# Kernel optimization log

Measured on AMD Instinct MI355X. Metric: run time of the kernel, lower is better.

## Reference

```python
import jax, jax.numpy as jnp
import numpy as np

B, N, D, K = 16, 1024, 512, 8
NUM_ITERS = 3
EPS = 1e-08
LN_EPS = 1e-05


def layer_norm(x, g, b):
    m = jnp.mean(x, axis=-1, keepdims=True)
    v = jnp.var(x, axis=-1, keepdims=True)
    return (x - m) * jax.lax.rsqrt(v + LN_EPS) * g + b


def setup_inputs() -> dict:
    key = jax.random.key(0)
    ks = jax.random.split(key, 8)
    s = 1.0 / np.sqrt(D)
    return {
        "embeddings": jax.random.normal(ks[0], (B, N, D), jnp.float32),
        "noise_init": jax.random.normal(ks[1], (B, K, D), jnp.float32),
        "noise_final": jax.random.normal(ks[2], (B, K, D), jnp.float32),
        "slots_mu": jax.random.normal(ks[3], (1, K, D), jnp.float32) * s,
        "slots_logsigma": jax.random.normal(ks[4], (1, K, D), jnp.float32) * s,
        "mixing_coeffs": jnp.ones((1, K), jnp.float32) / K,
        "Wk": jax.random.normal(ks[5], (D, D), jnp.float32) * s,
        "bk": jnp.zeros((D,), jnp.float32),
        "Wq": jax.random.normal(ks[6], (D, D), jnp.float32) * s,
        "bq": jnp.zeros((D,), jnp.float32),
        "Wv": jax.random.normal(ks[7], (D, D), jnp.float32) * s,
        "bv": jnp.zeros((D,), jnp.float32),
        "ln_g": jnp.ones((D,), jnp.float32),
        "ln_b": jnp.zeros((D,), jnp.float32),
    }


def reference(embeddings, noise_init, noise_final, slots_mu, slots_logsigma,
              mixing_coeffs, Wk, bk, Wq, bq, Wv, bv, ln_g, ln_b):
    b, n, d = embeddings.shape
    mixing = jnp.broadcast_to(mixing_coeffs, (b, K))           # [B,K]
    mu = jnp.broadcast_to(slots_mu, (b, K, d))                 # [B,K,D]
    sigma = jnp.exp(jnp.broadcast_to(slots_logsigma, (b, K, d)))
    slots = mu + sigma * noise_init                            # sampled slots

    x = layer_norm(embeddings, ln_g, ln_b)
    keys = x @ Wk + bk                                         # [B,N,D]
    values = x @ Wv + bv                                       # [B,N,D]
    # slots are never updated inside the loop, so queries are loop-invariant
    queries = slots @ Wq + bq                                  # [B,K,D]

    log2pi = jnp.float32(np.log(2.0 * np.pi))
    attn = None
    for _ in range(NUM_ITERS):
        diff = keys[:, :, None, :] - queries[:, None, :, :]    # [B,N,K,D]
        gll = -0.5 * jnp.sum(diff * diff / (sigma[:, None] ** 2 + EPS), axis=-1)  # [B,N,K]
        gll = (-0.5 * d * log2pi
               - 0.5 * jnp.sum(jnp.log(jnp.abs(sigma) + EPS), axis=-1)[:, None, :]
               + gll)
        attn = mixing[:, None, :] * gll                        # [B,N,K]
        attn = attn / jnp.sum(attn, axis=-1, keepdims=True)
        attn = attn / (jnp.sum(attn, axis=1, keepdims=True) + EPS)
        mu = jnp.einsum('bnk,bnd->bkd', attn, values)          # [B,K,D]
        diff2 = values[:, :, None, :] - mu[:, None, :, :]      # [B,N,K,D]
        sigma = jnp.einsum('bnk,bnkd->bkd', attn, diff2 * diff2)
        mixing = jnp.sum(attn, axis=1) / n

    sigma = jnp.maximum(jnp.abs(sigma), EPS)
    slots = mu + sigma * noise_final
    return slots, jnp.transpose(attn, (0, 2, 1))
```

## Files before the change

kernel.cpp:

```cpp
#include <hip/hip_runtime.h>
#include <math.h>

#define BB 16
#define NN 1024
#define DD 512
#define KK 8
#define EPS_ 1e-8f
#define LN_EPS_ 1e-5f
#define GLL_C0 (-470.4965290007924f)

typedef __attribute__((ext_vector_type(8))) short short8;
typedef __attribute__((ext_vector_type(4))) short short4v;
typedef __attribute__((ext_vector_type(4))) float f32x4;
typedef __attribute__((ext_vector_type(4))) int int4v;

static __device__ inline short f2bf(float f) {
    unsigned u = __builtin_bit_cast(unsigned, f);
    u = (u + 0x7fff + ((u >> 16) & 1)) >> 16;
    return (short)u;
}
static __device__ inline float bf2f(short s) {
    unsigned u = ((unsigned)(unsigned short)s) << 16;
    return __builtin_bit_cast(float, u);
}

struct Params {
    const float *emb, *noise_init, *noise_final, *slots_mu, *slots_logsg,
                *mixing_co, *Wk, *bk, *Wq, *bq, *Wv, *bv, *ln_g, *ln_b;
    float *out;
    float *queries, *attn, *s1p, *s2p, *off, *mix16, *colsum;
    short *Abf, *E, *Vbf, *WtKV, *WqT, *slotbf, *F_bt;
};

__global__ __launch_bounds__(256) void k_pre(Params p)
{
    __shared__ __align__(16) short eb[4352];
    int u = blockIdx.x, tid = threadIdx.x;
    if (u < 4096) {
        int row  = u * 4 + (tid >> 6);
        int lane = tid & 63;
        const float* e = p.emb + (size_t)row * DD + lane * 8;
        float4 v0 = *(const float4*)e;
        float4 v1 = *(const float4*)(e + 4);
        float v[8] = {v0.x, v0.y, v0.z, v0.w, v1.x, v1.y, v1.z, v1.w};
        float s = 0.0f;
#pragma unroll
        for (int j = 0; j < 8; j++) s += v[j];
#pragma unroll
        for (int off = 32; off; off >>= 1) s += __shfl_xor(s, off);
        float m = s * (1.0f / DD);
        float vs = 0.0f;
#pragma unroll
        for (int j = 0; j < 8; j++) { float d = v[j] - m; vs = fmaf(d, d, vs); }
#pragma unroll
        for (int off = 32; off; off >>= 1) vs += __shfl_xor(vs, off);
        float rstd = rsqrtf(vs * (1.0f / DD) + LN_EPS_);

        float4 g0 = *(const float4*)&p.ln_g[lane * 8];
        float4 g1 = *(const float4*)&p.ln_g[lane * 8 + 4];
        float4 b0 = *(const float4*)&p.ln_b[lane * 8];
        float4 b1 = *(const float4*)&p.ln_b[lane * 8 + 4];
        float g[8] = {g0.x, g0.y, g0.z, g0.w, g1.x, g1.y, g1.z, g1.w};
        float bb[8] = {b0.x, b0.y, b0.z, b0.w, b1.x, b1.y, b1.z, b1.w};
        short8 o;
#pragma unroll
        for (int j = 0; j < 8; j++) o[j] = f2bf(fmaf((v[j] - m) * rstd, g[j], bb[j]));
        *(short8*)&p.Abf[(size_t)row * DD + lane * 8] = o;
    } else if (u < 4864) {
        int idx = u - 4096;
        int z = idx >> 8, rem = idx & 255;
        const float* W = (z == 0) ? p.Wk : (z == 1) ? p.Wv : p.Wq;
        short* T; int nbase;
        if (z < 2) { T = p.WtKV; nbase = z * 512; } else { T = p.WqT; nbase = 0; }
        int k0 = (rem & 15) * 32, n0 = (rem >> 4) * 32;
        int tx = tid & 31, ty = tid >> 5;
        float (*t)[33] = (float (*)[33])eb;
#pragma unroll
        for (int q = 0; q < 4; q++)
            t[ty + q * 8][tx] = W[(size_t)(k0 + ty + q * 8) * DD + n0 + tx];
        __syncthreads();
#pragma unroll
        for (int q = 0; q < 4; q++)
            T[(size_t)(nbase + n0 + ty + q * 8) * DD + k0 + tx] = f2bf(t[tx][ty + q * 8]);
    } else {
        int idx = u - 4864;
        int b = idx >> 3, k = idx & 7;
#pragma unroll
        for (int q = 0; q < 2; q++) {
            int d = tid + q * 256;
            float sg = expf(p.slots_logsg[k * DD + d]);
            float sl = fmaf(sg, p.noise_init[((size_t)(b * KK + k)) * DD + d],
                            p.slots_mu[k * DD + d]);
            p.slotbf[((size_t)(b * KK + k)) * DD + d] = f2bf(sl);
        }
    }
}

__global__ __launch_bounds__(256) void k_gemm(Params p)
{
    __shared__ __align__(16) short smem[16384];
    int u = blockIdx.x, tid = threadIdx.x;
    int w = tid >> 6, l = tid & 63;
    int x, by, qmode;
    if (u >= 1024) { qmode = 1; x = u - 1024; if (x >= 4) return; by = 128; }
    else           { qmode = 0; x = u >> 7;   by = u & 127; }
    const short* A  = qmode ? p.slotbf : p.Abf + (size_t)by * 128 * DD;
    const short* Bt = qmode ? p.WqT : p.WtKV;
    int row0 = qmode ? 0 : by * 128;
    int col0 = x * 128;

    short* As = smem;
    short* Bs = smem + 8192;
    int sr = l >> 3;
    int sg_off = ((l & 7) ^ sr) * 8;
    int mq = (w & 1) * 64, nq = (w >> 1) * 64;
    int fr = l & 15;
    int orow = (l >> 4) * 4, ocol = l & 15;

    int4v ra[4], rb4[4];
    auto LOADR = [&](int k0) {
#pragma unroll
        for (int j = 0; j < 4; j++) {
            int rbj = w * 32 + j * 8;
            int r   = rbj + sr;
            ra[j]  = *(const int4v*)(A  + (size_t)r * DD + k0 + sg_off);
            rb4[j] = *(const int4v*)(Bt + (size_t)(col0 + r) * DD + k0 + sg_off);
        }
    };
    auto WRITES = [&]() {
#pragma unroll
        for (int j = 0; j < 4; j++) {
            int rbj = w * 32 + j * 8;
            *(int4v*)&As[rbj * 64 + l * 8] = ra[j];
            *(int4v*)&Bs[rbj * 64 + l * 8] = rb4[j];
        }
    };

    f32x4 acc[4][4] = {};
    LOADR(0);
    WRITES();
    __syncthreads();
    for (int i = 0; i < 8; i++) {
        if (i < 7) LOADR((i + 1) * 64);
#pragma unroll
        for (int kk = 0; kk < 2; kk++) {
            int g = kk * 4 + (l >> 4);
            short8 af[4], bfv[4];
#pragma unroll
            for (int mi = 0; mi < 4; mi++)
                af[mi] = *(const short8*)&As[(mq + mi * 16 + fr) * 64 + (g ^ (fr & 7)) * 8];
#pragma unroll
            for (int ni = 0; ni < 4; ni++)
                bfv[ni] = *(const short8*)&Bs[(nq + ni * 16 + fr) * 64 + (g ^ (fr & 7)) * 8];
#pragma unroll
            for (int mi = 0; mi < 4; mi++)
#pragma unroll
                for (int ni = 0; ni < 4; ni++)
                    acc[mi][ni] = __builtin_amdgcn_mfma_f32_16x16x32_bf16(
                        af[mi], bfv[ni], acc[mi][ni], 0, 0, 0);
        }
        __syncthreads();
        if (i < 7) {
            WRITES();
            __syncthreads();
        }
    }

    float bvv[4];
#pragma unroll
    for (int ni = 0; ni < 4; ni++) {
        int col = col0 + nq + ni * 16 + ocol;
        bvv[ni] = qmode ? p.bq[col] : (x < 4 ? p.bk[col] : p.bv[col - 512]);
    }

    if (qmode) {
#pragma unroll
        for (int ni = 0; ni < 4; ni++) {
            int col = col0 + nq + ni * 16 + ocol;
#pragma unroll
            for (int mi = 0; mi < 4; mi++)
#pragma unroll
                for (int r = 0; r < 4; r++)
                    p.queries[(size_t)(mq + mi * 16 + orow + r) * DD + col] =
                        acc[mi][ni][r] + bvv[ni];
        }
    } else {
        short* eb = smem;
        int npass = (x < 4) ? 2 : 1;
        for (int pass = 0; pass < npass; pass++) {
#pragma unroll
            for (int mi = 0; mi < 4; mi++)
#pragma unroll
                for (int r = 0; r < 4; r++) {
                    int row = mq + mi * 16 + orow + r;
                    int sw = ((row >> 2) & 3) << 1;
#pragma unroll
                    for (int ni = 0; ni < 4; ni++) {
                        int colg = nq + ni * 16 + ocol;
                        float val = acc[mi][ni][r] + bvv[ni];
                        if (x < 4 && pass == 0) val = val * val;
                        eb[row * 128 + (((colg >> 3) ^ sw) * 8) + (colg & 7)] = f2bf(val);
                    }
                }
            __syncthreads();
#pragma unroll
            for (int i = 0; i < 8; i++) {
                int row = i * 16 + w * 4 + (l >> 4);
                int c = l & 15;
                int cc = c ^ (((row >> 2) & 3) << 1);
                short8 vv = *(const short8*)&eb[row * 128 + cc * 8];
                if (x < 4) {
                    size_t a = (size_t)(row0 + row) * 1024 +
                               (pass ? 512 + col0 : col0) + c * 8;
                    *(short8*)&p.E[a] = vv;
                } else {
                    *(short8*)&p.Vbf[(size_t)(row0 + row) * 512 +
                                     (col0 - 512) + c * 8] = vv;
                }
            }
            __syncthreads();
        }
    }
}

__global__ __launch_bounds__(256) void k_fprep0(Params p)
{
    __shared__ float red[512];
    int u = blockIdx.x, tid = threadIdx.x;
    int b = u >> 4, k = u & 15;
    short* Fr = p.F_bt + (size_t)(b * 16 + k) * 1024;
    if (k >= KK) {
        short4v zv = {0, 0, 0, 0};
        *(short4v*)&Fr[tid * 4] = zv;
        if (tid == 0) { p.off[b * 16 + k] = 0.0f; p.mix16[b * 16 + k] = 0.0f; }
        return;
    }
    float* rc = red;
    float* rl = red + 256;
    float c = 0.0f, ld = 0.0f;
#pragma unroll
    for (int q = 0; q < 2; q++) {
        int d = tid * 2 + q;
        float sg = expf(p.slots_logsg[k * DD + d]);
        float iv = 1.0f / (sg * sg + EPS_);
        float qv = p.queries[((size_t)(b * KK + k)) * DD + d];
        Fr[d]       = f2bf(-0.5f * iv);
        Fr[512 + d] = f2bf(qv * iv);
        c  = fmaf(qv * qv, iv, c);
        ld += logf(fabsf(sg) + EPS_);
    }
    rc[tid] = c; rl[tid] = ld;
    __syncthreads();
    for (int s = 128; s > 0; s >>= 1) {
        if (tid < s) { rc[tid] += rc[tid + s]; rl[tid] += rl[tid + s]; }
        __syncthreads();
    }
    if (tid == 0) {
        p.off[b * 16 + k]    = GLL_C0 - 0.5f * rl[0] - 0.5f * rc[0];
        p.mix16[b * 16 + k]  = p.mixing_co[k];
        p.colsum[b * KK + k] = 0.0f;
    }
}

__global__ __launch_bounds__(256) void k_gllmu(Params p)
{
    __shared__ f32x4 red[2][64];
    __shared__ float asml[32 * KK];
    int u = blockIdx.x, tid = threadIdx.x;
    int w = tid >> 6, l = tid & 63;
    int b = u >> 5, chunk = u & 31;
    int n0 = chunk * 32;
    int t = w & 1, khalf = w >> 1;

    const short* Ea = p.E + ((size_t)(b * NN + n0 + t * 16 + (l & 15))) * 1024
                      + khalf * 512 + (l >> 4) * 8;
    const short* Fa = p.F_bt + (size_t)(b * 16 + (l & 15)) * 1024
                      + khalf * 512 + (l >> 4) * 8;
    f32x4 acc0 = {}, acc1 = {};
#pragma unroll
    for (int j = 0; j < 8; j++) {
        short8 a0 = *(const short8*)&Ea[j * 64];
        short8 f0 = *(const short8*)&Fa[j * 64];
        acc0 = __builtin_amdgcn_mfma_f32_16x16x32_bf16(a0, f0, acc0, 0, 0, 0);
        short8 a1 = *(const short8*)&Ea[j * 64 + 32];
        short8 f1 = *(const short8*)&Fa[j * 64 + 32];
        acc1 = __builtin_amdgcn_mfma_f32_16x16x32_bf16(a1, f1, acc1, 0, 0, 0);
    }
    f32x4 acc = acc0 + acc1;

    if (khalf) red[t][l] = acc;
    __syncthreads();
    if (!khalf) {
        acc += red[t][l];
        int col = l & 15;
        int rloc = t * 16 + (l >> 4) * 4;
        float offv = p.off[b * 16 + col];
        float mixv = p.mix16[b * 16 + col];
        float a[4], den[4];
#pragma unroll
        for (int r = 0; r < 4; r++) {
            a[r] = mixv * (acc[r] + offv);
            den[r] = a[r];
        }
#pragma unroll
        for (int mask = 1; mask <= 8; mask <<= 1)
#pragma unroll
            for (int r = 0; r < 4; r++) den[r] += __shfl_xor(den[r], mask);
        float csl = 0.0f;
        if (col < KK) {
#pragma unroll
            for (int r = 0; r < 4; r++) {
                float vv = a[r] / den[r];
                asml[(rloc + r) * KK + col] = vv;
                p.attn[((size_t)(b * NN + n0 + rloc + r)) * KK + col] = vv;
                csl += vv;
            }
        }
        csl += __shfl_xor(csl, 16);
        csl += __shfl_xor(csl, 32);
        if (l < KK) atomicAdd(&p.colsum[b * KK + l], csl);
    }
    __syncthreads();

    int d0 = tid * 2;
    float s1[2][KK] = {}, s2[2][KK] = {};
    const short* vb = p.Vbf + ((size_t)(b * NN + n0)) * DD + d0;
#pragma unroll 4
    for (int nn = 0; nn < 32; nn++) {
        short2 vs = *(const short2*)&vb[(size_t)nn * DD];
        float v0 = bf2f(vs.x), v1 = bf2f(vs.y);
        float v0q = v0 * v0, v1q = v1 * v1;
        float4 a0 = *(const float4*)&asml[nn * KK];
        float4 a1 = *(const float4*)&asml[nn * KK + 4];
        float aa[8] = {a0.x, a0.y, a0.z, a0.w, a1.x, a1.y, a1.z, a1.w};
#pragma unroll
        for (int k = 0; k < KK; k++) {
            s1[0][k] = fmaf(aa[k], v0, s1[0][k]);
            s2[0][k] = fmaf(aa[k], v0q, s2[0][k]);
            s1[1][k] = fmaf(aa[k], v1, s1[1][k]);
            s2[1][k] = fmaf(aa[k], v1q, s2[1][k]);
        }
    }
    size_t base = ((size_t)(b * 32 + chunk) * KK) * DD + d0;
#pragma unroll
    for (int k = 0; k < KK; k++) {
        *(float2*)&p.s1p[base + (size_t)k * DD] = make_float2(s1[0][k], s1[1][k]);
        *(float2*)&p.s2p[base + (size_t)k * DD] = make_float2(s2[0][k], s2[1][k]);
    }
}

__global__ __launch_bounds__(256) void k_fprep(Params p)
{
    __shared__ float red[512];
    int u = blockIdx.x, tid = threadIdx.x;
    int b = u >> 3, k = u & 7;
    float cs   = p.colsum[b * KK + k];
    float inv  = 1.0f / (cs + EPS_);
    float ssum = cs * inv;
    short* Fr = p.F_bt + (size_t)(b * 16 + k) * 1024;
    float* rc = red;
    float* rl = red + 256;
    float c = 0.0f, ld = 0.0f;
#pragma unroll
    for (int q = 0; q < 2; q++) {
        int d = tid * 2 + q;
        float s1 = 0.0f, s2 = 0.0f;
#pragma unroll
        for (int ns = 0; ns < 32; ns++) {
            size_t o = ((size_t)(b * 32 + ns) * KK + k) * DD + d;
            s1 += p.s1p[o];
            s2 += p.s2p[o];
        }
        float m  = s1 * inv;
        float sg = s2 * inv - m * m * (2.0f - ssum);
        float iv = 1.0f / (sg * sg + EPS_);
        float qv = p.queries[((size_t)(b * KK + k)) * DD + d];
        Fr[d]       = f2bf(-0.5f * iv);
        Fr[512 + d] = f2bf(qv * iv);
        c  = fmaf(qv * qv, iv, c);
        ld += logf(fabsf(sg) + EPS_);
    }
    rc[tid] = c; rl[tid] = ld;
    __syncthreads();
    for (int s = 128; s > 0; s >>= 1) {
        if (tid < s) { rc[tid] += rc[tid + s]; rl[tid] += rl[tid + s]; }
        __syncthreads();
    }
    if (tid == 0) {
        p.off[b * 16 + k]    = GLL_C0 - 0.5f * rl[0] - 0.5f * rc[0];
        p.mix16[b * 16 + k]  = ssum * (1.0f / NN);
        p.colsum[b * KK + k] = 0.0f;
    }
}

__global__ __launch_bounds__(256) void k_final(Params p)
{
    int u = blockIdx.x, tid = threadIdx.x;
    if (u < 256) {
        int gid = u * 256 + tid;
        int d = gid & 511;
        int k = (gid >> 9) & 7;
        int b = gid >> 12;
        float s1 = 0.0f, s2 = 0.0f;
#pragma unroll
        for (int ns = 0; ns < 32; ns++) {
            size_t o = ((size_t)(b * 32 + ns) * KK + k) * DD + d;
            s1 += p.s1p[o];
            s2 += p.s2p[o];
        }
        float cs   = p.colsum[b * KK + k];
        float inv  = 1.0f / (cs + EPS_);
        float ssum = cs * inv;
        float m    = s1 * inv;
        float sg   = s2 * inv - m * m * (2.0f - ssum);
        p.out[gid] = fmaf(fmaxf(fabsf(sg), EPS_), p.noise_final[gid], m);
    } else {
        int gid = (u - 256) * 256 + tid;
        int b = gid >> 13;
        int k = (gid >> 10) & 7;
        int n = gid & 1023;
        float cs = p.colsum[b * KK + k];
        p.out[BB * KK * DD + gid] =
            p.attn[((size_t)(b * NN + n)) * KK + k] / (cs + EPS_);
    }
}

extern "C" void kernel_launch(void* const* d_in, const int* in_sizes, int n_in,
                              void* d_out, int out_size, void* d_ws, size_t ws_size,
                              hipStream_t stream)
{
    Params pp;
    pp.emb         = (const float*)d_in[0];
    pp.noise_init  = (const float*)d_in[1];
    pp.noise_final = (const float*)d_in[2];
    pp.slots_mu    = (const float*)d_in[3];
    pp.slots_logsg = (const float*)d_in[4];
    pp.mixing_co   = (const float*)d_in[5];
    pp.Wk          = (const float*)d_in[6];
    pp.bk          = (const float*)d_in[7];
    pp.Wq          = (const float*)d_in[8];
    pp.bq          = (const float*)d_in[9];
    pp.Wv          = (const float*)d_in[10];
    pp.bv          = (const float*)d_in[11];
    pp.ln_g        = (const float*)d_in[12];
    pp.ln_b        = (const float*)d_in[13];
    pp.out         = (float*)d_out;

    float* ws = (float*)d_ws;
    pp.queries = ws;
    pp.attn    = pp.queries + BB * KK * DD;
    pp.s1p     = pp.attn + BB * NN * KK;
    pp.s2p     = pp.s1p + (size_t)BB * 32 * KK * DD;
    pp.off     = pp.s2p + (size_t)BB * 32 * KK * DD;
    pp.mix16   = pp.off + BB * 16;
    pp.colsum  = pp.mix16 + BB * 16;
    pp.Abf     = (short*)(pp.colsum + BB * KK);
    pp.E       = pp.Abf + (size_t)BB * NN * DD;
    pp.Vbf     = pp.E + (size_t)BB * NN * 1024;
    pp.WtKV    = pp.Vbf + (size_t)BB * NN * DD;
    pp.WqT     = pp.WtKV + (size_t)1024 * DD;
    pp.slotbf  = pp.WqT + (size_t)DD * DD;
    pp.F_bt    = pp.slotbf + (size_t)BB * KK * DD;

    k_pre<<<4992, 256, 0, stream>>>(pp);
    k_gemm<<<1032, 256, 0, stream>>>(pp);
    k_fprep0<<<256, 256, 0, stream>>>(pp);
    for (int it = 0; it < 3; it++) {
        k_gllmu<<<512, 256, 0, stream>>>(pp);
        if (it < 2) k_fprep<<<128, 256, 0, stream>>>(pp);
    }
    k_final<<<768, 256, 0, stream>>>(pp);
}
```

Baseline: 229.8 us.

## Store keys once and square them in the GLL kernel; load GEMM fragments directly

The GEMM no longer writes an expanded [K^2 | K] bf16 buffer. It writes only K, and the GLL kernel squares the loaded key fragments in registers before the MFMA. This halves the key-side writes and the reads repeated across the three iterations. The GEMM main loop also drops LDS staging and barriers, loading MFMA fragments straight from global memory with register double buffering. The direct loads are uncoalesced 16-byte row reads and may rely on cache hits. Squaring a bf16-rounded key adds a little rounding difference.

```diff
diff --git a/kernel.cpp b/kernel.cpp
--- a/kernel.cpp
+++ b/kernel.cpp
@@ -12,7 +12,6 @@
 typedef __attribute__((ext_vector_type(8))) short short8;
 typedef __attribute__((ext_vector_type(4))) short short4v;
 typedef __attribute__((ext_vector_type(4))) float f32x4;
-typedef __attribute__((ext_vector_type(4))) int int4v;
 
 static __device__ inline short f2bf(float f) {
     unsigned u = __builtin_bit_cast(unsigned, f);
@@ -29,7 +28,7 @@
                 *mixing_co, *Wk, *bk, *Wq, *bq, *Wv, *bv, *ln_g, *ln_b;
     float *out;
     float *queries, *attn, *s1p, *s2p, *off, *mix16, *colsum;
-    short *Abf, *E, *Vbf, *WtKV, *WqT, *slotbf, *F_bt;
+    short *Abf, *Kbf, *Vbf, *WtKV, *WqT, *slotbf, *F_bt;
 };
 
 __global__ __launch_bounds__(256) void k_pre(Params p)
@@ -98,7 +97,7 @@
 
 __global__ __launch_bounds__(256) void k_gemm(Params p)
 {
-    __shared__ __align__(16) short smem[16384];
+    __shared__ __align__(16) short eb[128 * 128];
     int u = blockIdx.x, tid = threadIdx.x;
     int w = tid >> 6, l = tid & 63;
     int x, by, qmode;
@@ -109,61 +108,39 @@
     int row0 = qmode ? 0 : by * 128;
     int col0 = x * 128;
 
-    short* As = smem;
-    short* Bs = smem + 8192;
-    int sr = l >> 3;
-    int sg_off = ((l & 7) ^ sr) * 8;
     int mq = (w & 1) * 64, nq = (w >> 1) * 64;
     int fr = l & 15;
     int orow = (l >> 4) * 4, ocol = l & 15;
 
-    int4v ra[4], rb4[4];
-    auto LOADR = [&](int k0) {
-#pragma unroll
-        for (int j = 0; j < 4; j++) {
-            int rbj = w * 32 + j * 8;
-            int r   = rbj + sr;
-            ra[j]  = *(const int4v*)(A  + (size_t)r * DD + k0 + sg_off);
-            rb4[j] = *(const int4v*)(Bt + (size_t)(col0 + r) * DD + k0 + sg_off);
-        }
-    };
-    auto WRITES = [&]() {
-#pragma unroll
-        for (int j = 0; j < 4; j++) {
-            int rbj = w * 32 + j * 8;
-            *(int4v*)&As[rbj * 64 + l * 8] = ra[j];
-            *(int4v*)&Bs[rbj * 64 + l * 8] = rb4[j];
-        }
-    };
-
+    const short* Abase = A + (size_t)(mq + fr) * DD + (l >> 4) * 8;
+    const short* Bbase = Bt + (size_t)(col0 + nq + fr) * DD + (l >> 4) * 8;
+
+    short8 af[2][4], bf[2][4];
     f32x4 acc[4][4] = {};
-    LOADR(0);
-    WRITES();
-    __syncthreads();
-    for (int i = 0; i < 8; i++) {
-        if (i < 7) LOADR((i + 1) * 64);
-#pragma unroll
-        for (int kk = 0; kk < 2; kk++) {
-            int g = kk * 4 + (l >> 4);
-            short8 af[4], bfv[4];
+
+#pragma unroll
+    for (int mi = 0; mi < 4; mi++) af[0][mi] = *(const short8*)(Abase + (size_t)mi * 16 * DD);
+#pragma unroll
+    for (int ni = 0; ni < 4; ni++) bf[0][ni] = *(const short8*)(Bbase + (size_t)ni * 16 * DD);
+
+#pragma unroll
+    for (int ks = 0; ks < 16; ks++) {
+        int cur = ks & 1;
+        if (ks < 15) {
+            int ko = (ks + 1) * 32;
 #pragma unroll
             for (int mi = 0; mi < 4; mi++)
-                af[mi] = *(const short8*)&As[(mq + mi * 16 + fr) * 64 + (g ^ (fr & 7)) * 8];
+                af[cur ^ 1][mi] = *(const short8*)(Abase + (size_t)mi * 16 * DD + ko);
 #pragma unroll
             for (int ni = 0; ni < 4; ni++)
-                bfv[ni] = *(const short8*)&Bs[(nq + ni * 16 + fr) * 64 + (g ^ (fr & 7)) * 8];
-#pragma unroll
-            for (int mi = 0; mi < 4; mi++)
-#pragma unroll
-                for (int ni = 0; ni < 4; ni++)
-                    acc[mi][ni] = __builtin_amdgcn_mfma_f32_16x16x32_bf16(
-                        af[mi], bfv[ni], acc[mi][ni], 0, 0, 0);
-        }
-        __syncthreads();
-        if (i < 7) {
-            WRITES();
-            __syncthreads();
-        }
+                bf[cur ^ 1][ni] = *(const short8*)(Bbase + (size_t)ni * 16 * DD + ko);
+        }
+#pragma unroll
+        for (int mi = 0; mi < 4; mi++)
+#pragma unroll
+            for (int ni = 0; ni < 4; ni++)
+                acc[mi][ni] = __builtin_amdgcn_mfma_f32_16x16x32_bf16(
+                    af[cur][mi], bf[cur][ni], acc[mi][ni], 0, 0, 0);
     }
 
     float bvv[4];
@@ -185,40 +162,29 @@
                         acc[mi][ni][r] + bvv[ni];
         }
     } else {
-        short* eb = smem;
-        int npass = (x < 4) ? 2 : 1;
-        for (int pass = 0; pass < npass; pass++) {
-#pragma unroll
-            for (int mi = 0; mi < 4; mi++)
-#pragma unroll
-                for (int r = 0; r < 4; r++) {
-                    int row = mq + mi * 16 + orow + r;
-                    int sw = ((row >> 2) & 3) << 1;
-#pragma unroll
-                    for (int ni = 0; ni < 4; ni++) {
-                        int colg = nq + ni * 16 + ocol;
-                        float val = acc[mi][ni][r] + bvv[ni];
-                        if (x < 4 && pass == 0) val = val * val;
-                        eb[row * 128 + (((colg >> 3) ^ sw) * 8) + (colg & 7)] = f2bf(val);
-                    }
-                }
-            __syncthreads();
-#pragma unroll
-            for (int i = 0; i < 8; i++) {
-                int row = i * 16 + w * 4 + (l >> 4);
-                int c = l & 15;
-                int cc = c ^ (((row >> 2) & 3) << 1);
-                short8 vv = *(const short8*)&eb[row * 128 + cc * 8];
-                if (x < 4) {
-                    size_t a = (size_t)(row0 + row) * 1024 +
-                               (pass ? 512 + col0 : col0) + c * 8;
-                    *(short8*)&p.E[a] = vv;
-                } else {
-                    *(short8*)&p.Vbf[(size_t)(row0 + row) * 512 +
-                                     (col0 - 512) + c * 8] = vv;
+        short* dst = (x < 4) ? p.Kbf : p.Vbf;
+        int ccol0 = (x & 3) * 128;
+#pragma unroll
+        for (int mi = 0; mi < 4; mi++)
+#pragma unroll
+            for (int r = 0; r < 4; r++) {
+                int row = mq + mi * 16 + orow + r;
+                int sw = ((row >> 2) & 3) << 1;
+#pragma unroll
+                for (int ni = 0; ni < 4; ni++) {
+                    int colg = nq + ni * 16 + ocol;
+                    eb[row * 128 + (((colg >> 3) ^ sw) * 8) + (colg & 7)] =
+                        f2bf(acc[mi][ni][r] + bvv[ni]);
                 }
             }
-            __syncthreads();
+        __syncthreads();
+#pragma unroll
+        for (int i = 0; i < 8; i++) {
+            int row = i * 16 + w * 4 + (l >> 4);
+            int c = l & 15;
+            int cc = c ^ (((row >> 2) & 3) << 1);
+            short8 vv = *(const short8*)&eb[row * 128 + cc * 8];
+            *(short8*)&dst[(size_t)(row0 + row) * 512 + ccol0 + c * 8] = vv;
         }
     }
 }
@@ -272,19 +238,24 @@
     int n0 = chunk * 32;
     int t = w & 1, khalf = w >> 1;
 
-    const short* Ea = p.E + ((size_t)(b * NN + n0 + t * 16 + (l & 15))) * 1024
-                      + khalf * 512 + (l >> 4) * 8;
-    const short* Fa = p.F_bt + (size_t)(b * 16 + (l & 15)) * 1024
-                      + khalf * 512 + (l >> 4) * 8;
+    const short* Ka = p.Kbf + ((size_t)(b * NN + n0 + t * 16 + (l & 15))) * 512
+                      + khalf * 256 + (l >> 4) * 8;
+    const short* Fi = p.F_bt + (size_t)(b * 16 + (l & 15)) * 1024
+                      + khalf * 256 + (l >> 4) * 8;
     f32x4 acc0 = {}, acc1 = {};
 #pragma unroll
     for (int j = 0; j < 8; j++) {
-        short8 a0 = *(const short8*)&Ea[j * 64];
-        short8 f0 = *(const short8*)&Fa[j * 64];
-        acc0 = __builtin_amdgcn_mfma_f32_16x16x32_bf16(a0, f0, acc0, 0, 0, 0);
-        short8 a1 = *(const short8*)&Ea[j * 64 + 32];
-        short8 f1 = *(const short8*)&Fa[j * 64 + 32];
-        acc1 = __builtin_amdgcn_mfma_f32_16x16x32_bf16(a1, f1, acc1, 0, 0, 0);
+        short8 kf = *(const short8*)&Ka[j * 32];
+        short8 f0 = *(const short8*)&Fi[j * 32];
+        short8 f1 = *(const short8*)&Fi[j * 32 + 512];
+        short8 k2;
+#pragma unroll
+        for (int e = 0; e < 8; e++) {
+            float kv = bf2f(kf[e]);
+            k2[e] = f2bf(kv * kv);
+        }
+        acc0 = __builtin_amdgcn_mfma_f32_16x16x32_bf16(k2, f0, acc0, 0, 0, 0);
+        acc1 = __builtin_amdgcn_mfma_f32_16x16x32_bf16(kf, f1, acc1, 0, 0, 0);
     }
     f32x4 acc = acc0 + acc1;
 
@@ -455,8 +426,8 @@
     pp.mix16   = pp.off + BB * 16;
     pp.colsum  = pp.mix16 + BB * 16;
     pp.Abf     = (short*)(pp.colsum + BB * KK);
-    pp.E       = pp.Abf + (size_t)BB * NN * DD;
-    pp.Vbf     = pp.E + (size_t)BB * NN * 1024;
+    pp.Kbf     = pp.Abf + (size_t)BB * NN * DD;
+    pp.Vbf     = pp.Kbf + (size_t)BB * NN * DD;
     pp.WtKV    = pp.Vbf + (size_t)BB * NN * DD;
     pp.WqT     = pp.WtKV + (size_t)1024 * DD;
     pp.slotbf  = pp.WqT + (size_t)DD * DD;
```

Result: slower. 250.5 us (+9.0%).

## Store keys once in bf16 and square them on the fly in the GLL kernel

Applied to the files above, without the earlier changes.

The GEMM epilogue now writes only the bf16 keys (512 columns) instead of an interleaved [k^2, k] buffer of 1024 columns. The key square is recomputed inside k_gllmu from the loaded bf16 key before the MFMA. This halves the key buffer written by the GEMM and read in each of the three iterations. k_gllmu also moves to 512 threads: four waves split the D dimension, with a three-way shared-memory reduction, and the mu/sigma accumulation uses one column per thread. Squaring the already-rounded bf16 key adds a small precision change, plus extra ALU conversion work per load.

```diff
diff --git a/kernel.cpp b/kernel.cpp
--- a/kernel.cpp
+++ b/kernel.cpp
@@ -29,7 +29,7 @@
                 *mixing_co, *Wk, *bk, *Wq, *bq, *Wv, *bv, *ln_g, *ln_b;
     float *out;
     float *queries, *attn, *s1p, *s2p, *off, *mix16, *colsum;
-    short *Abf, *E, *Vbf, *WtKV, *WqT, *slotbf, *F_bt;
+    short *Abf, *Kbf, *Vbf, *WtKV, *WqT, *slotbf, *F_bt;
 };
 
 __global__ __launch_bounds__(256) void k_pre(Params p)
@@ -186,39 +186,29 @@
         }
     } else {
         short* eb = smem;
-        int npass = (x < 4) ? 2 : 1;
-        for (int pass = 0; pass < npass; pass++) {
-#pragma unroll
-            for (int mi = 0; mi < 4; mi++)
-#pragma unroll
-                for (int r = 0; r < 4; r++) {
-                    int row = mq + mi * 16 + orow + r;
-                    int sw = ((row >> 2) & 3) << 1;
-#pragma unroll
-                    for (int ni = 0; ni < 4; ni++) {
-                        int colg = nq + ni * 16 + ocol;
-                        float val = acc[mi][ni][r] + bvv[ni];
-                        if (x < 4 && pass == 0) val = val * val;
-                        eb[row * 128 + (((colg >> 3) ^ sw) * 8) + (colg & 7)] = f2bf(val);
-                    }
-                }
-            __syncthreads();
-#pragma unroll
-            for (int i = 0; i < 8; i++) {
-                int row = i * 16 + w * 4 + (l >> 4);
-                int c = l & 15;
-                int cc = c ^ (((row >> 2) & 3) << 1);
-                short8 vv = *(const short8*)&eb[row * 128 + cc * 8];
-                if (x < 4) {
-                    size_t a = (size_t)(row0 + row) * 1024 +
-                               (pass ? 512 + col0 : col0) + c * 8;
-                    *(short8*)&p.E[a] = vv;
-                } else {
-                    *(short8*)&p.Vbf[(size_t)(row0 + row) * 512 +
-                                     (col0 - 512) + c * 8] = vv;
+        short* dst = (x < 4) ? p.Kbf : p.Vbf;
+        int ccol0 = (x & 3) * 128;
+#pragma unroll
+        for (int mi = 0; mi < 4; mi++)
+#pragma unroll
+            for (int r = 0; r < 4; r++) {
+                int row = mq + mi * 16 + orow + r;
+                int sw = ((row >> 2) & 3) << 1;
+#pragma unroll
+                for (int ni = 0; ni < 4; ni++) {
+                    int colg = nq + ni * 16 + ocol;
+                    eb[row * 128 + (((colg >> 3) ^ sw) * 8) + (colg & 7)] =
+                        f2bf(acc[mi][ni][r] + bvv[ni]);
                 }
             }
-            __syncthreads();
+        __syncthreads();
+#pragma unroll
+        for (int i = 0; i < 8; i++) {
+            int row = i * 16 + w * 4 + (l >> 4);
+            int c = l & 15;
+            int cc = c ^ (((row >> 2) & 3) << 1);
+            short8 vv = *(const short8*)&eb[row * 128 + cc * 8];
+            *(short8*)&dst[(size_t)(row0 + row) * 512 + ccol0 + c * 8] = vv;
         }
     }
 }
@@ -262,36 +252,42 @@
     }
 }
 
-__global__ __launch_bounds__(256) void k_gllmu(Params p)
-{
-    __shared__ f32x4 red[2][64];
+__global__ __launch_bounds__(512) void k_gllmu(Params p)
+{
+    __shared__ f32x4 red[3][2][64];
     __shared__ float asml[32 * KK];
     int u = blockIdx.x, tid = threadIdx.x;
     int w = tid >> 6, l = tid & 63;
     int b = u >> 5, chunk = u & 31;
     int n0 = chunk * 32;
-    int t = w & 1, khalf = w >> 1;
-
-    const short* Ea = p.E + ((size_t)(b * NN + n0 + t * 16 + (l & 15))) * 1024
-                      + khalf * 512 + (l >> 4) * 8;
-    const short* Fa = p.F_bt + (size_t)(b * 16 + (l & 15)) * 1024
-                      + khalf * 512 + (l >> 4) * 8;
+    int t = w & 1, ks = w >> 1;
+
+    const short* Ka = p.Kbf + ((size_t)(b * NN + n0 + t * 16 + (l & 15))) * 512
+                      + ks * 128 + (l >> 4) * 8;
+    const short* Fi = p.F_bt + (size_t)(b * 16 + (l & 15)) * 1024
+                      + ks * 128 + (l >> 4) * 8;
     f32x4 acc0 = {}, acc1 = {};
 #pragma unroll
-    for (int j = 0; j < 8; j++) {
-        short8 a0 = *(const short8*)&Ea[j * 64];
-        short8 f0 = *(const short8*)&Fa[j * 64];
-        acc0 = __builtin_amdgcn_mfma_f32_16x16x32_bf16(a0, f0, acc0, 0, 0, 0);
-        short8 a1 = *(const short8*)&Ea[j * 64 + 32];
-        short8 f1 = *(const short8*)&Fa[j * 64 + 32];
-        acc1 = __builtin_amdgcn_mfma_f32_16x16x32_bf16(a1, f1, acc1, 0, 0, 0);
+    for (int j = 0; j < 4; j++) {
+        short8 kf = *(const short8*)&Ka[j * 32];
+        short8 f0 = *(const short8*)&Fi[j * 32];
+        short8 f1 = *(const short8*)&Fi[j * 32 + 512];
+        short8 k2;
+#pragma unroll
+        for (int e = 0; e < 8; e++) {
+            float kv = bf2f(kf[e]);
+            k2[e] = f2bf(kv * kv);
+        }
+        acc0 = __builtin_amdgcn_mfma_f32_16x16x32_bf16(k2, f0, acc0, 0, 0, 0);
+        acc1 = __builtin_amdgcn_mfma_f32_16x16x32_bf16(kf, f1, acc1, 0, 0, 0);
     }
     f32x4 acc = acc0 + acc1;
 
-    if (khalf) red[t][l] = acc;
+    if (ks) red[ks - 1][t][l] = acc;
     __syncthreads();
-    if (!khalf) {
-        acc += red[t][l];
+    if (ks == 0) {
+#pragma unroll
+        for (int i = 0; i < 3; i++) acc += red[i][t][l];
         int col = l & 15;
         int rloc = t * 16 + (l >> 4) * 4;
         float offv = p.off[b * 16 + col];
@@ -322,30 +318,26 @@
     }
     __syncthreads();
 
-    int d0 = tid * 2;
-    float s1[2][KK] = {}, s2[2][KK] = {};
-    const short* vb = p.Vbf + ((size_t)(b * NN + n0)) * DD + d0;
+    float s1[KK] = {}, s2[KK] = {};
+    const short* vb = p.Vbf + ((size_t)(b * NN + n0)) * DD + tid;
 #pragma unroll 4
     for (int nn = 0; nn < 32; nn++) {
-        short2 vs = *(const short2*)&vb[(size_t)nn * DD];
-        float v0 = bf2f(vs.x), v1 = bf2f(vs.y);
-        float v0q = v0 * v0, v1q = v1 * v1;
+        float v = bf2f(vb[(size_t)nn * DD]);
+        float vq = v * v;
         float4 a0 = *(const float4*)&asml[nn * KK];
         float4 a1 = *(const float4*)&asml[nn * KK + 4];
         float aa[8] = {a0.x, a0.y, a0.z, a0.w, a1.x, a1.y, a1.z, a1.w};
 #pragma unroll
         for (int k = 0; k < KK; k++) {
-            s1[0][k] = fmaf(aa[k], v0, s1[0][k]);
-            s2[0][k] = fmaf(aa[k], v0q, s2[0][k]);
-            s1[1][k] = fmaf(aa[k], v1, s1[1][k]);
-            s2[1][k] = fmaf(aa[k], v1q, s2[1][k]);
-        }
-    }
-    size_t base = ((size_t)(b * 32 + chunk) * KK) * DD + d0;
+            s1[k] = fmaf(aa[k], v, s1[k]);
+            s2[k] = fmaf(aa[k], vq, s2[k]);
+        }
+    }
+    size_t base = ((size_t)(b * 32 + chunk) * KK) * DD + tid;
 #pragma unroll
     for (int k = 0; k < KK; k++) {
-        *(float2*)&p.s1p[base + (size_t)k * DD] = make_float2(s1[0][k], s1[1][k]);
-        *(float2*)&p.s2p[base + (size_t)k * DD] = make_float2(s2[0][k], s2[1][k]);
+        p.s1p[base + (size_t)k * DD] = s1[k];
+        p.s2p[base + (size_t)k * DD] = s2[k];
     }
 }
 
@@ -455,8 +447,8 @@
     pp.mix16   = pp.off + BB * 16;
     pp.colsum  = pp.mix16 + BB * 16;
     pp.Abf     = (short*)(pp.colsum + BB * KK);
-    pp.E       = pp.Abf + (size_t)BB * NN * DD;
-    pp.Vbf     = pp.E + (size_t)BB * NN * 1024;
+    pp.Kbf     = pp.Abf + (size_t)BB * NN * DD;
+    pp.Vbf     = pp.Kbf + (size_t)BB * NN * DD;
     pp.WtKV    = pp.Vbf + (size_t)BB * NN * DD;
     pp.WqT     = pp.WtKV + (size_t)1024 * DD;
     pp.slotbf  = pp.WqT + (size_t)DD * DD;
@@ -466,7 +458,7 @@
     k_gemm<<<1032, 256, 0, stream>>>(pp);
     k_fprep0<<<256, 256, 0, stream>>>(pp);
     for (int it = 0; it < 3; it++) {
-        k_gllmu<<<512, 256, 0, stream>>>(pp);
+        k_gllmu<<<512, 512, 0, stream>>>(pp);
         if (it < 2) k_fprep<<<128, 256, 0, stream>>>(pp);
     }
     k_final<<<768, 256, 0, stream>>>(pp);
```

New measurement: 203.5 us. 1.13x faster.
